# Kernel tuning notes

Hardware: AMD Instinct MI355X
Metric: run time of the kernel (lower is better)

Reference implementation:

```python
import jax, jax.numpy as jnp
import numpy as np

B, S, D, H, FF = 2, 4096, 512, 8, 2048
HD = D // H
EPS = 1e-5


def setup_inputs() -> dict:
    key = jax.random.key(0)
    ks = jax.random.split(key, 14)
    init = lambda k, shape: jax.random.normal(k, shape, dtype=jnp.float32) * 0.02
    return {
        "x": jax.random.normal(ks[0], (B, S, D), dtype=jnp.float32),
        "Wq": init(ks[1], (D, D)), "bq": jnp.zeros((D,), jnp.float32),
        "Wk": init(ks[2], (D, D)), "bk": jnp.zeros((D,), jnp.float32),
        "Wv": init(ks[3], (D, D)), "bv": jnp.zeros((D,), jnp.float32),
        "Wo": init(ks[4], (D, D)), "bo": jnp.zeros((D,), jnp.float32),
        "W1": init(ks[5], (D, FF)), "b1": jnp.zeros((FF,), jnp.float32),
        "W2": init(ks[6], (FF, D)), "b2": jnp.zeros((D,), jnp.float32),
        "g1": jnp.ones((D,), jnp.float32), "beta1": jnp.zeros((D,), jnp.float32),
        "g2": jnp.ones((D,), jnp.float32), "beta2": jnp.zeros((D,), jnp.float32),
    }


def layer_norm(x, g, b):
    mu = jnp.mean(x, axis=-1, keepdims=True)
    var = jnp.mean(jnp.square(x - mu), axis=-1, keepdims=True)
    return (x - mu) * jax.lax.rsqrt(var + EPS) * g + b


def reference(x, Wq, bq, Wk, bk, Wv, bv, Wo, bo, W1, b1, W2, b2, g1, beta1, g2, beta2):
    # --- pre-LN self-attention block ---
    residual = x
    h = layer_norm(x, g1, beta1)
    # project and split heads: [B, H, S, HD]
    q = (h @ Wq + bq).reshape(B, S, H, HD).transpose(0, 2, 1, 3)
    k = (h @ Wk + bk).reshape(B, S, H, HD).transpose(0, 2, 1, 3)
    v = (h @ Wv + bv).reshape(B, S, H, HD).transpose(0, 2, 1, 3)
    scale = HD ** -0.5
    scores = jnp.einsum('bhqd,bhkd->bhqk', q, k) * scale  # [B,H,S,S] materialized
    attn = jax.nn.softmax(scores, axis=-1)
    ctx = jnp.einsum('bhqk,bhkd->bhqd', attn, v)
    ctx = ctx.transpose(0, 2, 1, 3).reshape(B, S, D)
    attn_out = ctx @ Wo + bo
    x = residual + attn_out  # dropout p=0.0 -> identity
    # --- pre-LN FFN block ---
    residual = x
    h = layer_norm(x, g2, beta2)
    h = jax.nn.gelu(h @ W1 + b1, approximate=False)  # nn.GELU default = exact erf
    h = h @ W2 + b2
    x = residual + h
    return (x, attn)
```

## Files before the change

### kernel.cpp

```cpp
#include <hip/hip_runtime.h>
#include <hip/hip_bf16.h>

#define B_ 2
#define S_ 4096
#define D_ 512
#define H_ 8
#define HD_ 64
#define FF_ 2048
#define NT_ (B_*S_)
#define EPS_ 1e-5f

typedef __attribute__((ext_vector_type(8))) short bf16x8;
typedef __attribute__((ext_vector_type(4))) float f32x4;
typedef __attribute__((ext_vector_type(4))) unsigned int u32x4;

__device__ __forceinline__ short f2bf(float f){
  __hip_bfloat16 h = __float2bfloat16(f);
  return __builtin_bit_cast(short, h);
}
__device__ __forceinline__ float bf2f(short s){
  return __bfloat162float(__builtin_bit_cast(__hip_bfloat16, s));
}
__device__ __forceinline__ unsigned pack2(float lo, float hi){
  return ((unsigned)(unsigned short)f2bf(hi) << 16) | (unsigned short)f2bf(lo);
}
__device__ __forceinline__ void load8(const float* p, float* f){
  f32x4 a = *(const f32x4*)p; f32x4 b = *(const f32x4*)(p+4);
  #pragma unroll
  for (int j=0;j<4;j++){ f[j]=a[j]; f[4+j]=b[j]; }
}
__device__ __forceinline__ void load8(const short* p, float* f){
  bf16x8 v = *(const bf16x8*)p;
  #pragma unroll
  for (int j=0;j<8;j++) f[j]=bf2f(v[j]);
}
__device__ __forceinline__ float ldval(const float* p, size_t i){ return p[i]; }
__device__ __forceinline__ float ldval(const short* p, size_t i){ return bf2f(p[i]); }
__device__ __forceinline__ void stval(float* p, size_t i, float v){ p[i]=v; }
__device__ __forceinline__ void stval(short* p, size_t i, float v){ p[i]=f2bf(v); }

#define GLL(src, dst) __builtin_amdgcn_global_load_lds( \
    (const __attribute__((address_space(1))) void*)(src), \
    (__attribute__((address_space(3))) void*)(dst), 16, 0, 0)

__global__ __launch_bounds__(256) void transpose_bf(const float* __restrict__ W,
                                                    short* __restrict__ WT, int K, int N){
  __shared__ float tile[32][33];
  int n0 = blockIdx.x*32, k0 = blockIdx.y*32;
  int tx = threadIdx.x, ty = threadIdx.y;
  #pragma unroll
  for (int i=0;i<32;i+=8)
    tile[ty+i][tx] = W[(size_t)(k0+ty+i)*N + n0+tx];
  __syncthreads();
  #pragma unroll
  for (int i=0;i<32;i+=8)
    WT[(size_t)(n0+ty+i)*K + k0+tx] = f2bf(tile[tx][ty+i]);
}

__global__ __launch_bounds__(256) void transpose_v(const short* __restrict__ V,
                                                   short* __restrict__ VT){
  __shared__ short tile[32][33];
  int d0 = blockIdx.x*32, s0 = blockIdx.y*32, bh = blockIdx.z;
  int b = bh >> 3, h = bh & (H_-1);
  const short* Vp = V + (size_t)b*S_*D_ + (size_t)h*HD_;
  short* VTp = VT + (size_t)bh*HD_*S_;
  int tx = threadIdx.x, ty = threadIdx.y;
  #pragma unroll
  for (int i=0;i<32;i+=8)
    tile[ty+i][tx] = Vp[(size_t)(s0+ty+i)*D_ + d0+tx];
  __syncthreads();
  #pragma unroll
  for (int i=0;i<32;i+=8)
    VTp[(size_t)(d0+ty+i)*S_ + s0+tx] = tile[tx][ty+i];
}

template<typename TIn>
__global__ __launch_bounds__(256) void ln_kernel(const TIn* __restrict__ X,
                                                 const float* __restrict__ G,
                                                 const float* __restrict__ Bt,
                                                 short* __restrict__ O){
  int wid = threadIdx.x>>6, lane = threadIdx.x&63;
  int tok = blockIdx.x*4 + wid;
  const TIn* xp = X + (size_t)tok*D_;
  float f[8]; load8(xp + lane*8, f);
  float s=0.f, s2=0.f;
  #pragma unroll
  for (int j=0;j<8;j++){ s+=f[j]; s2+=f[j]*f[j]; }
  #pragma unroll
  for (int m=1;m<64;m<<=1){ s += __shfl_xor(s,m); s2 += __shfl_xor(s2,m); }
  float mu = s*(1.f/D_);
  float var = s2*(1.f/D_) - mu*mu;
  float rr = rsqrtf(var + EPS_);
  f32x4 g0 = *(const f32x4*)(G + lane*8), g1v = *(const f32x4*)(G + lane*8 + 4);
  f32x4 b0 = *(const f32x4*)(Bt + lane*8), b1v = *(const f32x4*)(Bt + lane*8 + 4);
  bf16x8 o;
  #pragma unroll
  for (int j=0;j<4;j++){
    o[j]   = f2bf((f[j]-mu)*rr*g0[j]  + b0[j]);
    o[4+j] = f2bf((f[4+j]-mu)*rr*g1v[j] + b1v[j]);
  }
  *(bf16x8*)(O + (size_t)tok*D_ + lane*8) = o;
}

template<int EPI, typename TR, typename TO>
__global__ __launch_bounds__(256) void gemm_bt(const short* __restrict__ A,
                                               const short* __restrict__ BT,
                                               const float* __restrict__ bias,
                                               const TR* __restrict__ res,
                                               TO* __restrict__ out,
                                               int M, int N, int K){
  __shared__ __align__(16) short As[128*64];
  __shared__ __align__(16) short Bs[128*64];
  int m0 = blockIdx.y*128, n0 = blockIdx.x*128;
  int tid = threadIdx.x, lane = tid&63, wid = tid>>6;
  int wr = wid>>1, wc = wid&1;
  int r = lane&15, qh = lane>>4;
  int srow = wid*32 + (lane>>3);
  int scole = ((lane&7)*8);
  f32x4 zero = {0.f,0.f,0.f,0.f};
  f32x4 acc[4][4];
  #pragma unroll
  for (int i=0;i<4;i++)
    #pragma unroll
    for (int j=0;j<4;j++) acc[i][j] = zero;

  for (int k0=0;k0<K;k0+=64){
    __syncthreads();
    #pragma unroll
    for (int i=0;i<4;i++){
      int row = srow + i*8;
      int cole = scole ^ ((row&7)*8);
      GLL(&A [(size_t)(m0+row)*K + k0 + cole], As + (size_t)(wid*32+i*8)*64);
      GLL(&BT[(size_t)(n0+row)*K + k0 + cole], Bs + (size_t)(wid*32+i*8)*64);
    }
    __syncthreads();
    #pragma unroll
    for (int half=0; half<2; half++){
      bf16x8 a[4], b[4];
      #pragma unroll
      for (int i=0;i<4;i++){
        int ar = wr*64+i*16+r;
        a[i] = *(const bf16x8*)((const char*)As + (size_t)ar*128 + ((qh*16+half*64) ^ ((ar&7)*16)));
        int br = wc*64+i*16+r;
        b[i] = *(const bf16x8*)((const char*)Bs + (size_t)br*128 + ((qh*16+half*64) ^ ((br&7)*16)));
      }
      #pragma unroll
      for (int mi=0;mi<4;mi++)
        #pragma unroll
        for (int ni=0;ni<4;ni++)
          acc[mi][ni] = __builtin_amdgcn_mfma_f32_16x16x32_bf16(a[mi], b[ni], acc[mi][ni], 0,0,0);
    }
  }
  #pragma unroll
  for (int mi=0;mi<4;mi++){
    #pragma unroll
    for (int ni=0;ni<4;ni++){
      int col = n0 + wc*64 + ni*16 + r;
      float bs = bias[col];
      #pragma unroll
      for (int j=0;j<4;j++){
        int row = m0 + wr*64 + mi*16 + (lane>>4)*4 + j;
        float v = acc[mi][ni][j] + bs;
        if (EPI==1) v += ldval(res, (size_t)row*N + col);
        if (EPI==2) v = 0.5f*v*(1.f + erff(v*0.70710678118f));
        stval(out, (size_t)row*N + col, v);
      }
    }
  }
}

__global__ __launch_bounds__(256, 4) void attn_s1(const short* __restrict__ Q,
                                                  const short* __restrict__ Kt,
                                                  float* __restrict__ dinv){
  __shared__ __align__(16) char smem[32768];
  __shared__ float dcomb[4][4][16];
  int wid = threadIdx.x>>6, lane = threadIdx.x&63;
  int bh = blockIdx.y, b = bh>>3, h = bh&7;
  int q0 = blockIdx.x*64;
  int koff = wid*1024;
  int r = lane&15, qh = lane>>4;
  const short* Qp = Q  + (size_t)b*S_*D_ + (size_t)h*HD_;
  const short* Kp = Kt + (size_t)b*S_*D_ + (size_t)h*HD_;

  char* stg = smem + wid*8192;
  short* KB0 = (short*)stg;  short* KB1 = (short*)(stg+4096);

  auto stageK = [&](int sc, short* buf){
    #pragma unroll
    for (int i=0;i<4;i++){
      int row = i*8 + (lane>>3);
      int col = ((lane&7)*8) ^ ((row&7)*8);
      GLL(&Kp[(size_t)(sc+row)*D_ + col], buf + i*512);
    }
  };
  const int kc0 = (qh*16) ^ ((r&7)<<4);
  const int kc1 = (64 + qh*16) ^ ((r&7)<<4);

  bf16x8 aq[4][2];
  #pragma unroll
  for (int qt=0;qt<4;qt++){
    aq[qt][0] = *(const bf16x8*)&Qp[(size_t)(q0+qt*16+r)*D_ + qh*8];
    aq[qt][1] = *(const bf16x8*)&Qp[(size_t)(q0+qt*16+r)*D_ + 32 + qh*8];
  }
  const f32x4 zero = {0.f,0.f,0.f,0.f};
  float part[4] = {0.f,0.f,0.f,0.f};

#define S1BODY(n, NW, DOSTG) { \
  asm volatile("s_waitcnt vmcnt(" #NW ")" ::: "memory"); \
  short* kb_ = ((n)&1)? KB1 : KB0; \
  bf16x8 kf0 = *(const bf16x8*)((char*)kb_ + r*128 + kc0); \
  bf16x8 kf1 = *(const bf16x8*)((char*)kb_ + r*128 + kc1); \
  bf16x8 kf2 = *(const bf16x8*)((char*)kb_ + (16+r)*128 + kc0); \
  bf16x8 kf3 = *(const bf16x8*)((char*)kb_ + (16+r)*128 + kc1); \
  asm volatile("s_waitcnt lgkmcnt(0)" ::: "memory"); \
  if (DOSTG) stageK(koff + ((n)+2)*32, kb_); \
  _Pragma("unroll") \
  for (int qt=0;qt<4;qt++){ \
    f32x4 s0 = __builtin_amdgcn_mfma_f32_16x16x32_bf16(kf0, aq[qt][0], zero, 0,0,0); \
    s0 = __builtin_amdgcn_mfma_f32_16x16x32_bf16(kf1, aq[qt][1], s0, 0,0,0); \
    f32x4 s1 = __builtin_amdgcn_mfma_f32_16x16x32_bf16(kf2, aq[qt][0], zero, 0,0,0); \
    s1 = __builtin_amdgcn_mfma_f32_16x16x32_bf16(kf3, aq[qt][1], s1, 0,0,0); \
    _Pragma("unroll") \
    for (int j=0;j<4;j++) part[qt] += __expf(s0[j]*0.125f) + __expf(s1[j]*0.125f); \
  } \
}

  stageK(koff, KB0); stageK(koff+32, KB1);
  S1BODY(0,4,1)
  for (int k2=0;k2<14;k2++){ S1BODY(2*k2+1,4,1) S1BODY(2*k2+2,4,1) }
  S1BODY(29,4,1) S1BODY(30,4,0) S1BODY(31,0,0)
#undef S1BODY

  #pragma unroll
  for (int qt=0;qt<4;qt++){
    part[qt] += __shfl_xor(part[qt],16);
    part[qt] += __shfl_xor(part[qt],32);
  }
  if (lane < 16){
    #pragma unroll
    for (int qt=0;qt<4;qt++) dcomb[wid][qt][r] = part[qt];
  }
  __syncthreads();
  if (wid == 0){
    int qt = lane>>4, rr = lane&15;
    float s = dcomb[0][qt][rr]+dcomb[1][qt][rr]+dcomb[2][qt][rr]+dcomb[3][qt][rr];
    dinv[(size_t)bh*S_ + q0 + qt*16 + rr] = 1.f/s;
  }
}

__global__ __launch_bounds__(256, 2) void attn_s2(const short* __restrict__ Q,
                                                  const short* __restrict__ Kt,
                                                  const short* __restrict__ VT,
                                                  const float* __restrict__ dinv,
                                                  float* __restrict__ attn_o,
                                                  short* __restrict__ ctx){
  __shared__ __align__(16) char smem[65536];
  int wid = threadIdx.x>>6, lane = threadIdx.x&63;
  int bh = blockIdx.y, b = bh>>3, h = bh&7;
  int q0 = blockIdx.x*64;
  int koff = wid*1024;
  int r = lane&15, qh = lane>>4;
  bool hi4 = (lane>>4)&1, hi5 = (lane>>5)&1;
  const short* Qp = Q  + (size_t)b*S_*D_ + (size_t)h*HD_;
  const short* Kp = Kt + (size_t)b*S_*D_ + (size_t)h*HD_;
  const short* Vp = VT + (size_t)bh*HD_*S_;
  float* Ap = attn_o + (size_t)bh*S_*S_;

  char* stg = smem + wid*16384;
  short* KB0 = (short*)stg;         short* KB1 = (short*)(stg+4096);
  short* VB0 = (short*)(stg+8192);  short* VB1 = (short*)(stg+12288);

  auto stageK = [&](int sc, short* buf){
    #pragma unroll
    for (int i=0;i<4;i++){
      int row = i*8 + (lane>>3);
      int col = ((lane&7)*8) ^ ((row&7)*8);
      GLL(&Kp[(size_t)(sc+row)*D_ + col], buf + i*512);
    }
  };
  auto stageV = [&](int sc, short* buf){
    #pragma unroll
    for (int i=0;i<4;i++){
      int d = i*16 + (lane>>2);
      int col = ((lane&3)*8) ^ ((d&3)*8);
      GLL(&Vp[(size_t)d*S_ + sc + col], buf + i*512);
    }
  };
  const int kc0 = (qh*16) ^ ((r&7)<<4);
  const int kc1 = (64 + qh*16) ^ ((r&7)<<4);
  const int vc  = (qh*16) ^ ((r&3)<<4);

  float invl[4];
  #pragma unroll
  for (int qt=0;qt<4;qt++) invl[qt] = dinv[(size_t)bh*S_ + q0 + qt*16 + r];

  bf16x8 aq[4][2];
  #pragma unroll
  for (int qt=0;qt<4;qt++){
    aq[qt][0] = *(const bf16x8*)&Qp[(size_t)(q0+qt*16+r)*D_ + qh*8];
    aq[qt][1] = *(const bf16x8*)&Qp[(size_t)(q0+qt*16+r)*D_ + 32 + qh*8];
  }
  const f32x4 zero = {0.f,0.f,0.f,0.f};

  f32x4 cacc[4][4];
  #pragma unroll
  for (int qt=0;qt<4;qt++)
    #pragma unroll
    for (int n2=0;n2<4;n2++) cacc[qt][n2] = zero;

#define S2BODY(n, NW, DOSTG) { \
  asm volatile("s_waitcnt vmcnt(" #NW ")" ::: "memory"); \
  short* kb_ = ((n)&1)? KB1 : KB0; \
  short* vb_ = ((n)&1)? VB1 : VB0; \
  int sc_ = koff + (n)*32; \
  bf16x8 kf0 = *(const bf16x8*)((char*)kb_ + r*128 + kc0); \
  bf16x8 kf1 = *(const bf16x8*)((char*)kb_ + r*128 + kc1); \
  bf16x8 kf2 = *(const bf16x8*)((char*)kb_ + (16+r)*128 + kc0); \
  bf16x8 kf3 = *(const bf16x8*)((char*)kb_ + (16+r)*128 + kc1); \
  bf16x8 vf0 = *(const bf16x8*)((char*)vb_ + (r)*64    + vc); \
  bf16x8 vf1 = *(const bf16x8*)((char*)vb_ + (16+r)*64 + vc); \
  bf16x8 vf2 = *(const bf16x8*)((char*)vb_ + (32+r)*64 + vc); \
  bf16x8 vf3 = *(const bf16x8*)((char*)vb_ + (48+r)*64 + vc); \
  asm volatile("s_waitcnt lgkmcnt(0)" ::: "memory"); \
  if (DOSTG){ stageK(koff+((n)+2)*32, kb_); stageV(koff+((n)+2)*32, vb_); } \
  _Pragma("unroll") \
  for (int qt=0;qt<4;qt++){ \
    f32x4 s0 = __builtin_amdgcn_mfma_f32_16x16x32_bf16(kf0, aq[qt][0], zero, 0,0,0); \
    s0 = __builtin_amdgcn_mfma_f32_16x16x32_bf16(kf1, aq[qt][1], s0, 0,0,0); \
    f32x4 s1 = __builtin_amdgcn_mfma_f32_16x16x32_bf16(kf2, aq[qt][0], zero, 0,0,0); \
    s1 = __builtin_amdgcn_mfma_f32_16x16x32_bf16(kf3, aq[qt][1], s1, 0,0,0); \
    float e0[4], e1[4]; \
    _Pragma("unroll") \
    for (int j=0;j<4;j++){ \
      e0[j] = __expf(s0[j]*0.125f)*invl[qt]; \
      e1[j] = __expf(s1[j]*0.125f)*invl[qt]; \
    } \
    f32x4 o0 = {e0[0],e0[1],e0[2],e0[3]}; \
    f32x4 o1 = {e1[0],e1[1],e1[2],e1[3]}; \
    float* dst = &Ap[(size_t)(q0+qt*16+r)*S_ + sc_ + qh*4]; \
    *(f32x4*)dst = o0; \
    *(f32x4*)(dst+16) = o1; \
    unsigned v0 = pack2(e0[0],e0[1]), v1 = pack2(e0[2],e0[3]); \
    unsigned v2 = pack2(e1[0],e1[1]), v3 = pack2(e1[2],e1[3]); \
    unsigned u0 = __shfl_xor((int)v0,16), u1 = __shfl_xor((int)v1,16); \
    unsigned u2 = __shfl_xor((int)v2,16), u3 = __shfl_xor((int)v3,16); \
    unsigned s0c0 = hi4?u0:v0, s0c1 = hi4?u1:v1, s0c2 = hi4?v0:u0, s0c3 = hi4?v1:u1; \
    unsigned s1c0 = hi4?u2:v2, s1c1 = hi4?u3:v3, s1c2 = hi4?v2:u2, s1c3 = hi4?v3:u3; \
    unsigned w0 = hi5?s0c0:s1c0, w1 = hi5?s0c1:s1c1, w2 = hi5?s0c2:s1c2, w3 = hi5?s0c3:s1c3; \
    unsigned wp0 = __shfl_xor((int)w0,32), wp1 = __shfl_xor((int)w1,32); \
    unsigned wp2 = __shfl_xor((int)w2,32), wp3 = __shfl_xor((int)w3,32); \
    u32x4 pw; \
    pw[0] = (qh==0)?s0c0:(qh==3)?s1c0:wp0; \
    pw[1] = (qh==0)?s0c1:(qh==3)?s1c1:wp1; \
    pw[2] = (qh==0)?s0c2:(qh==3)?s1c2:wp2; \
    pw[3] = (qh==0)?s0c3:(qh==3)?s1c3:wp3; \
    bf16x8 pa = __builtin_bit_cast(bf16x8, pw); \
    cacc[qt][0] = __builtin_amdgcn_mfma_f32_16x16x32_bf16(pa, vf0, cacc[qt][0], 0,0,0); \
    cacc[qt][1] = __builtin_amdgcn_mfma_f32_16x16x32_bf16(pa, vf1, cacc[qt][1], 0,0,0); \
    cacc[qt][2] = __builtin_amdgcn_mfma_f32_16x16x32_bf16(pa, vf2, cacc[qt][2], 0,0,0); \
    cacc[qt][3] = __builtin_amdgcn_mfma_f32_16x16x32_bf16(pa, vf3, cacc[qt][3], 0,0,0); \
  } \
}

  stageK(koff, KB0); stageV(koff, VB0);
  stageK(koff+32, KB1); stageV(koff+32, VB1);
  S2BODY(0,8,1)
  for (int k2=0;k2<14;k2++){ S2BODY(2*k2+1,16,1) S2BODY(2*k2+2,16,1) }
  S2BODY(29,16,1) S2BODY(30,16,0) S2BODY(31,8,0)
#undef S2BODY

  __syncthreads();
  float* cmb = (float*)smem;
  if (wid & 1){
    float* dstp = cmb + (wid>>1)*4096;
    #pragma unroll
    for (int qt=0;qt<4;qt++)
      #pragma unroll
      for (int n2=0;n2<4;n2++)
        #pragma unroll
        for (int j=0;j<4;j++)
          dstp[(qt*16+qh*4+j)*64 + n2*16 + r] = cacc[qt][n2][j];
  }
  __syncthreads();
  if (!(wid & 1)){
    float* srcp = cmb + (wid>>1)*4096;
    #pragma unroll
    for (int qt=0;qt<4;qt++)
      #pragma unroll
      for (int n2=0;n2<4;n2++)
        #pragma unroll
        for (int j=0;j<4;j++)
          cacc[qt][n2][j] += srcp[(qt*16+qh*4+j)*64 + n2*16 + r];
  }
  __syncthreads();
  if (wid == 2){
    #pragma unroll
    for (int qt=0;qt<4;qt++)
      #pragma unroll
      for (int n2=0;n2<4;n2++)
        #pragma unroll
        for (int j=0;j<4;j++)
          cmb[(qt*16+qh*4+j)*64 + n2*16 + r] = cacc[qt][n2][j];
  }
  __syncthreads();
  if (wid == 0){
    #pragma unroll
    for (int qt=0;qt<4;qt++)
      #pragma unroll
      for (int n2=0;n2<4;n2++)
        #pragma unroll
        for (int j=0;j<4;j++){
          float v = cacc[qt][n2][j] + cmb[(qt*16+qh*4+j)*64 + n2*16 + r];
          ctx[(size_t)(b*S_ + q0 + qt*16 + qh*4 + j)*D_ + h*HD_ + n2*16 + r] = f2bf(v);
        }
  }
}

extern "C" void kernel_launch(void* const* d_in, const int* in_sizes, int n_in,
                              void* d_out, int out_size, void* d_ws, size_t ws_size,
                              hipStream_t stream){
  const float* x   = (const float*)d_in[0];
  const float* Wq  = (const float*)d_in[1];
  const float* bq  = (const float*)d_in[2];
  const float* Wk  = (const float*)d_in[3];
  const float* bk  = (const float*)d_in[4];
  const float* Wv  = (const float*)d_in[5];
  const float* bv  = (const float*)d_in[6];
  const float* Wo  = (const float*)d_in[7];
  const float* bo  = (const float*)d_in[8];
  const float* W1  = (const float*)d_in[9];
  const float* b1  = (const float*)d_in[10];
  const float* W2  = (const float*)d_in[11];
  const float* b2  = (const float*)d_in[12];
  const float* g1  = (const float*)d_in[13];
  const float* be1 = (const float*)d_in[14];
  const float* g2  = (const float*)d_in[15];
  const float* be2 = (const float*)d_in[16];

  char* ws = (char*)d_ws;
  const size_t KB = 1024;
  short* wqT = (short*)(ws + 0*KB);
  short* wkT = (short*)(ws + 512*KB);
  short* wvT = (short*)(ws + 1024*KB);
  short* woT = (short*)(ws + 1536*KB);
  short* w1T = (short*)(ws + 2048*KB);
  short* w2T = (short*)(ws + 4096*KB);
  short* hbf = (short*)(ws + 6144*KB);
  short* Qb  = (short*)(ws + 14336*KB);
  short* Kb  = (short*)(ws + 22528*KB);
  short* Vb  = (short*)(ws + 30720*KB);
  short* VTb = (short*)(ws + 38912*KB);
  short* ctx = (short*)(ws + 47104*KB);
  float* dinv= (float*)(ws + 55296*KB);
  short* f1  = (short*)(ws + 14336*KB);

  float* out0 = (float*)d_out;
  float* attn = out0 + (size_t)NT_*D_;

  dim3 tb(32,8);
  transpose_bf<<<dim3(16,16),tb,0,stream>>>(Wq, wqT, 512, 512);
  transpose_bf<<<dim3(16,16),tb,0,stream>>>(Wk, wkT, 512, 512);
  transpose_bf<<<dim3(16,16),tb,0,stream>>>(Wv, wvT, 512, 512);
  transpose_bf<<<dim3(16,16),tb,0,stream>>>(Wo, woT, 512, 512);
  transpose_bf<<<dim3(64,16),tb,0,stream>>>(W1, w1T, 512, 2048);
  transpose_bf<<<dim3(16,64),tb,0,stream>>>(W2, w2T, 2048, 512);

  ln_kernel<float><<<NT_/4, 256, 0, stream>>>(x, g1, be1, hbf);

  gemm_bt<0,float,short><<<dim3(4,64),256,0,stream>>>(hbf, wqT, bq, nullptr, Qb, NT_, 512, 512);
  gemm_bt<0,float,short><<<dim3(4,64),256,0,stream>>>(hbf, wkT, bk, nullptr, Kb, NT_, 512, 512);
  gemm_bt<0,float,short><<<dim3(4,64),256,0,stream>>>(hbf, wvT, bv, nullptr, Vb, NT_, 512, 512);

  transpose_v<<<dim3(2,128,16),tb,0,stream>>>(Vb, VTb);

  attn_s1<<<dim3(64,16), 256, 0, stream>>>(Qb, Kb, dinv);
  attn_s2<<<dim3(64,16), 256, 0, stream>>>(Qb, Kb, VTb, dinv, attn, ctx);

  gemm_bt<1,float,float><<<dim3(4,64),256,0,stream>>>(ctx, woT, bo, x, out0, NT_, 512, 512);

  ln_kernel<float><<<NT_/4, 256, 0, stream>>>(out0, g2, be2, hbf);

  gemm_bt<2,float,short><<<dim3(16,64),256,0,stream>>>(hbf, w1T, b1, nullptr, f1, NT_, 2048, 512);

  gemm_bt<1,float,float><<<dim3(4,64),256,0,stream>>>(f1, w2T, b2, out0, out0, NT_, 512, 2048);
}
```

Before: 598.0 us.

## Fuse attention denominator pass and output pass into one 512-thread kernel

```diff
diff --git a/kernel.cpp b/kernel.cpp
--- a/kernel.cpp
+++ b/kernel.cpp
@@ -169,21 +169,27 @@
   }
 }
 
-__global__ __launch_bounds__(256, 4) void attn_s1(const short* __restrict__ Q,
-                                                  const short* __restrict__ Kt,
-                                                  float* __restrict__ dinv){
-  __shared__ __align__(16) char smem[32768];
-  __shared__ float dcomb[4][4][16];
+__global__ __launch_bounds__(512, 2) void attn_kernel(const short* __restrict__ Q,
+                                                      const short* __restrict__ Kt,
+                                                      const short* __restrict__ VT,
+                                                      float* __restrict__ attn_o,
+                                                      short* __restrict__ ctx){
+  __shared__ __align__(16) char smem[131072];
+  __shared__ float dcomb[8][8][16];
   int wid = threadIdx.x>>6, lane = threadIdx.x&63;
   int bh = blockIdx.y, b = bh>>3, h = bh&7;
-  int q0 = blockIdx.x*64;
-  int koff = wid*1024;
+  int q0 = blockIdx.x*128;
+  int koff = wid*512;
   int r = lane&15, qh = lane>>4;
+  bool hi4 = (lane>>4)&1, hi5 = (lane>>5)&1;
   const short* Qp = Q  + (size_t)b*S_*D_ + (size_t)h*HD_;
   const short* Kp = Kt + (size_t)b*S_*D_ + (size_t)h*HD_;
-
-  char* stg = smem + wid*8192;
-  short* KB0 = (short*)stg;  short* KB1 = (short*)(stg+4096);
+  const short* Vp = VT + (size_t)bh*HD_*S_;
+  float* Ap = attn_o + (size_t)bh*S_*S_;
+
+  char* stg = smem + wid*16384;
+  short* KB0 = (short*)stg;         short* KB1 = (short*)(stg+4096);
+  short* VB0 = (short*)(stg+8192);  short* VB1 = (short*)(stg+12288);
 
   auto stageK = [&](int sc, short* buf){
     #pragma unroll
@@ -193,17 +199,27 @@
       GLL(&Kp[(size_t)(sc+row)*D_ + col], buf + i*512);
     }
   };
+  auto stageV = [&](int sc, short* buf){
+    #pragma unroll
+    for (int i=0;i<4;i++){
+      int d = i*16 + (lane>>2);
+      int col = ((lane&3)*8) ^ ((d&3)*8);
+      GLL(&Vp[(size_t)d*S_ + sc + col], buf + i*512);
+    }
+  };
   const int kc0 = (qh*16) ^ ((r&7)<<4);
   const int kc1 = (64 + qh*16) ^ ((r&7)<<4);
-
-  bf16x8 aq[4][2];
-  #pragma unroll
-  for (int qt=0;qt<4;qt++){
+  const int vc  = (qh*16) ^ ((r&3)<<4);
+
+  bf16x8 aq[8][2];
+  #pragma unroll
+  for (int qt=0;qt<8;qt++){
     aq[qt][0] = *(const bf16x8*)&Qp[(size_t)(q0+qt*16+r)*D_ + qh*8];
     aq[qt][1] = *(const bf16x8*)&Qp[(size_t)(q0+qt*16+r)*D_ + 32 + qh*8];
   }
   const f32x4 zero = {0.f,0.f,0.f,0.f};
-  float part[4] = {0.f,0.f,0.f,0.f};
+
+  float part[8] = {0.f,0.f,0.f,0.f,0.f,0.f,0.f,0.f};
 
 #define S1BODY(n, NW, DOSTG) { \
   asm volatile("s_waitcnt vmcnt(" #NW ")" ::: "memory"); \
@@ -215,7 +231,7 @@
   asm volatile("s_waitcnt lgkmcnt(0)" ::: "memory"); \
   if (DOSTG) stageK(koff + ((n)+2)*32, kb_); \
   _Pragma("unroll") \
-  for (int qt=0;qt<4;qt++){ \
+  for (int qt=0;qt<8;qt++){ \
     f32x4 s0 = __builtin_amdgcn_mfma_f32_16x16x32_bf16(kf0, aq[qt][0], zero, 0,0,0); \
     s0 = __builtin_amdgcn_mfma_f32_16x16x32_bf16(kf1, aq[qt][1], s0, 0,0,0); \
     f32x4 s1 = __builtin_amdgcn_mfma_f32_16x16x32_bf16(kf2, aq[qt][0], zero, 0,0,0); \
@@ -227,84 +243,32 @@
 
   stageK(koff, KB0); stageK(koff+32, KB1);
   S1BODY(0,4,1)
-  for (int k2=0;k2<14;k2++){ S1BODY(2*k2+1,4,1) S1BODY(2*k2+2,4,1) }
-  S1BODY(29,4,1) S1BODY(30,4,0) S1BODY(31,0,0)
+  for (int k2=0;k2<6;k2++){ S1BODY(2*k2+1,4,1) S1BODY(2*k2+2,4,1) }
+  S1BODY(13,4,1) S1BODY(14,4,0) S1BODY(15,0,0)
 #undef S1BODY
 
   #pragma unroll
-  for (int qt=0;qt<4;qt++){
+  for (int qt=0;qt<8;qt++){
     part[qt] += __shfl_xor(part[qt],16);
     part[qt] += __shfl_xor(part[qt],32);
   }
   if (lane < 16){
     #pragma unroll
-    for (int qt=0;qt<4;qt++) dcomb[wid][qt][r] = part[qt];
-  }
-  __syncthreads();
-  if (wid == 0){
-    int qt = lane>>4, rr = lane&15;
-    float s = dcomb[0][qt][rr]+dcomb[1][qt][rr]+dcomb[2][qt][rr]+dcomb[3][qt][rr];
-    dinv[(size_t)bh*S_ + q0 + qt*16 + rr] = 1.f/s;
-  }
-}
-
-__global__ __launch_bounds__(256, 2) void attn_s2(const short* __restrict__ Q,
-                                                  const short* __restrict__ Kt,
-                                                  const short* __restrict__ VT,
-                                                  const float* __restrict__ dinv,
-                                                  float* __restrict__ attn_o,
-                                                  short* __restrict__ ctx){
-  __shared__ __align__(16) char smem[65536];
-  int wid = threadIdx.x>>6, lane = threadIdx.x&63;
-  int bh = blockIdx.y, b = bh>>3, h = bh&7;
-  int q0 = blockIdx.x*64;
-  int koff = wid*1024;
-  int r = lane&15, qh = lane>>4;
-  bool hi4 = (lane>>4)&1, hi5 = (lane>>5)&1;
-  const short* Qp = Q  + (size_t)b*S_*D_ + (size_t)h*HD_;
-  const short* Kp = Kt + (size_t)b*S_*D_ + (size_t)h*HD_;
-  const short* Vp = VT + (size_t)bh*HD_*S_;
-  float* Ap = attn_o + (size_t)bh*S_*S_;
-
-  char* stg = smem + wid*16384;
-  short* KB0 = (short*)stg;         short* KB1 = (short*)(stg+4096);
-  short* VB0 = (short*)(stg+8192);  short* VB1 = (short*)(stg+12288);
-
-  auto stageK = [&](int sc, short* buf){
-    #pragma unroll
-    for (int i=0;i<4;i++){
-      int row = i*8 + (lane>>3);
-      int col = ((lane&7)*8) ^ ((row&7)*8);
-      GLL(&Kp[(size_t)(sc+row)*D_ + col], buf + i*512);
-    }
-  };
-  auto stageV = [&](int sc, short* buf){
-    #pragma unroll
-    for (int i=0;i<4;i++){
-      int d = i*16 + (lane>>2);
-      int col = ((lane&3)*8) ^ ((d&3)*8);
-      GLL(&Vp[(size_t)d*S_ + sc + col], buf + i*512);
-    }
-  };
-  const int kc0 = (qh*16) ^ ((r&7)<<4);
-  const int kc1 = (64 + qh*16) ^ ((r&7)<<4);
-  const int vc  = (qh*16) ^ ((r&3)<<4);
-
-  float invl[4];
-  #pragma unroll
-  for (int qt=0;qt<4;qt++) invl[qt] = dinv[(size_t)bh*S_ + q0 + qt*16 + r];
-
-  bf16x8 aq[4][2];
-  #pragma unroll
-  for (int qt=0;qt<4;qt++){
-    aq[qt][0] = *(const bf16x8*)&Qp[(size_t)(q0+qt*16+r)*D_ + qh*8];
-    aq[qt][1] = *(const bf16x8*)&Qp[(size_t)(q0+qt*16+r)*D_ + 32 + qh*8];
-  }
-  const f32x4 zero = {0.f,0.f,0.f,0.f};
-
-  f32x4 cacc[4][4];
-  #pragma unroll
-  for (int qt=0;qt<4;qt++)
+    for (int qt=0;qt<8;qt++) dcomb[wid][qt][r] = part[qt];
+  }
+  __syncthreads();
+  float invl[8];
+  #pragma unroll
+  for (int qt=0;qt<8;qt++){
+    float s = 0.f;
+    #pragma unroll
+    for (int w=0;w<8;w++) s += dcomb[w][qt][r];
+    invl[qt] = 1.f/s;
+  }
+
+  f32x4 cacc[8][4];
+  #pragma unroll
+  for (int qt=0;qt<8;qt++)
     #pragma unroll
     for (int n2=0;n2<4;n2++) cacc[qt][n2] = zero;
 
@@ -324,7 +288,7 @@
   asm volatile("s_waitcnt lgkmcnt(0)" ::: "memory"); \
   if (DOSTG){ stageK(koff+((n)+2)*32, kb_); stageV(koff+((n)+2)*32, vb_); } \
   _Pragma("unroll") \
-  for (int qt=0;qt<4;qt++){ \
+  for (int qt=0;qt<8;qt++){ \
     f32x4 s0 = __builtin_amdgcn_mfma_f32_16x16x32_bf16(kf0, aq[qt][0], zero, 0,0,0); \
     s0 = __builtin_amdgcn_mfma_f32_16x16x32_bf16(kf1, aq[qt][1], s0, 0,0,0); \
     f32x4 s1 = __builtin_amdgcn_mfma_f32_16x16x32_bf16(kf2, aq[qt][0], zero, 0,0,0); \
@@ -365,16 +329,16 @@
   stageK(koff, KB0); stageV(koff, VB0);
   stageK(koff+32, KB1); stageV(koff+32, VB1);
   S2BODY(0,8,1)
-  for (int k2=0;k2<14;k2++){ S2BODY(2*k2+1,16,1) S2BODY(2*k2+2,16,1) }
-  S2BODY(29,16,1) S2BODY(30,16,0) S2BODY(31,8,0)
+  for (int k2=0;k2<6;k2++){ S2BODY(2*k2+1,24,1) S2BODY(2*k2+2,24,1) }
+  S2BODY(13,24,1) S2BODY(14,24,0) S2BODY(15,0,0)
 #undef S2BODY
 
   __syncthreads();
   float* cmb = (float*)smem;
   if (wid & 1){
-    float* dstp = cmb + (wid>>1)*4096;
-    #pragma unroll
-    for (int qt=0;qt<4;qt++)
+    float* dstp = cmb + (size_t)(wid>>1)*8192;
+    #pragma unroll
+    for (int qt=0;qt<8;qt++)
       #pragma unroll
       for (int n2=0;n2<4;n2++)
         #pragma unroll
@@ -383,9 +347,9 @@
   }
   __syncthreads();
   if (!(wid & 1)){
-    float* srcp = cmb + (wid>>1)*4096;
-    #pragma unroll
-    for (int qt=0;qt<4;qt++)
+    float* srcp = cmb + (size_t)(wid>>1)*8192;
+    #pragma unroll
+    for (int qt=0;qt<8;qt++)
       #pragma unroll
       for (int n2=0;n2<4;n2++)
         #pragma unroll
@@ -393,9 +357,31 @@
           cacc[qt][n2][j] += srcp[(qt*16+qh*4+j)*64 + n2*16 + r];
   }
   __syncthreads();
-  if (wid == 2){
-    #pragma unroll
-    for (int qt=0;qt<4;qt++)
+  if (!(wid & 1) && (wid & 2)){
+    float* dstp = cmb + (size_t)(wid>>2)*8192;
+    #pragma unroll
+    for (int qt=0;qt<8;qt++)
+      #pragma unroll
+      for (int n2=0;n2<4;n2++)
+        #pragma unroll
+        for (int j=0;j<4;j++)
+          dstp[(qt*16+qh*4+j)*64 + n2*16 + r] = cacc[qt][n2][j];
+  }
+  __syncthreads();
+  if (!(wid & 3)){
+    float* srcp = cmb + (size_t)(wid>>2)*8192;
+    #pragma unroll
+    for (int qt=0;qt<8;qt++)
+      #pragma unroll
+      for (int n2=0;n2<4;n2++)
+        #pragma unroll
+        for (int j=0;j<4;j++)
+          cacc[qt][n2][j] += srcp[(qt*16+qh*4+j)*64 + n2*16 + r];
+  }
+  __syncthreads();
+  if (wid == 4){
+    #pragma unroll
+    for (int qt=0;qt<8;qt++)
       #pragma unroll
       for (int n2=0;n2<4;n2++)
         #pragma unroll
@@ -405,7 +391,7 @@
   __syncthreads();
   if (wid == 0){
     #pragma unroll
-    for (int qt=0;qt<4;qt++)
+    for (int qt=0;qt<8;qt++)
       #pragma unroll
       for (int n2=0;n2<4;n2++)
         #pragma unroll
@@ -451,7 +437,6 @@
   short* Vb  = (short*)(ws + 30720*KB);
   short* VTb = (short*)(ws + 38912*KB);
   short* ctx = (short*)(ws + 47104*KB);
-  float* dinv= (float*)(ws + 55296*KB);
   short* f1  = (short*)(ws + 14336*KB);
 
   float* out0 = (float*)d_out;
@@ -473,8 +458,7 @@
 
   transpose_v<<<dim3(2,128,16),tb,0,stream>>>(Vb, VTb);
 
-  attn_s1<<<dim3(64,16), 256, 0, stream>>>(Qb, Kb, dinv);
-  attn_s2<<<dim3(64,16), 256, 0, stream>>>(Qb, Kb, VTb, dinv, attn, ctx);
+  attn_kernel<<<dim3(32,16), 512, 0, stream>>>(Qb, Kb, VTb, attn, ctx);
 
   gemm_bt<1,float,float><<<dim3(4,64),256,0,stream>>>(ctx, woT, bo, x, out0, NT_, 512, 512);
 
```

After: 767.9 us. 1.28x slower.
